# Optimization experiments

Hardware: AMD Instinct MI355X
Metric: run time of the kernel (lower is better)

The kernel has to match this reference:

```python
import jax, jax.numpy as jnp
import numpy as np

B, T, D_MODEL = 2, 2048, 2048
N_HEAD, N_KV, HD = 32, 8, 64


def _rope_tables(T, hd, base=10000.0):
    # standard rotary tables, (T, hd) with frequencies repeated over both halves
    inv_freq = 1.0 / (base ** (np.arange(0, hd // 2, dtype=np.float32) / (hd // 2)))
    t = np.arange(T, dtype=np.float32)
    freqs = np.outer(t, inv_freq)            # (T, hd/2)
    emb = np.concatenate([freqs, freqs], axis=-1)  # (T, hd)
    return jnp.asarray(np.cos(emb)), jnp.asarray(np.sin(emb))


def setup_inputs() -> dict:
    key = jax.random.key(0)
    ks = jax.random.split(key, 5)
    cos, sin = _rope_tables(T, HD)
    s = 0.02
    return {
        "x": jax.random.normal(ks[0], (B, T, D_MODEL), jnp.float32),
        "cos": cos,
        "sin": sin,
        "Wq": jax.random.normal(ks[1], (N_HEAD * HD, D_MODEL), jnp.float32) * s,
        "Wk": jax.random.normal(ks[2], (N_KV * HD, D_MODEL), jnp.float32) * s,
        "Wv": jax.random.normal(ks[3], (N_KV * HD, D_MODEL), jnp.float32) * s,
        "Wo": jax.random.normal(ks[4], (D_MODEL, N_HEAD * HD), jnp.float32) * s,
    }


def _apply_rope(x, cos, sin):
    # x: (B, H, T, D); cos/sin: (T, D)
    D = x.shape[-1]
    x1, x2 = x[..., : D // 2], x[..., D // 2 :]
    rot = jnp.concatenate([-x2, x1], axis=-1)
    c = cos[: x.shape[-2]][None, None]
    s = sin[: x.shape[-2]][None, None]
    return x * c + rot * s


def reference(x, cos, sin, Wq, Wk, Wv, Wo):
    Bv, Tv, _ = x.shape
    q = (x @ Wq.T).reshape(Bv, Tv, N_HEAD, HD).transpose(0, 2, 1, 3)  # (B,H,T,D)
    k = (x @ Wk.T).reshape(Bv, Tv, N_KV, HD).transpose(0, 2, 1, 3)    # (B,Hkv,T,D)
    v = (x @ Wv.T).reshape(Bv, Tv, N_KV, HD).transpose(0, 2, 1, 3)
    q = _apply_rope(q, cos, sin)
    k = _apply_rope(k, cos, sin)
    repeat = N_HEAD // N_KV
    if repeat > 1:
        k = jnp.repeat(k, repeat, axis=1)
        v = jnp.repeat(v, repeat, axis=1)
    scale = 1.0 / jnp.sqrt(jnp.float32(HD)).astype(x.dtype)
    scores = jnp.einsum("bhqd,bhkd->bhqk", q, k) * scale
    causal = jnp.tril(jnp.ones((Tv, Tv), dtype=bool))
    scores = jnp.where(causal[None, None], scores, jnp.finfo(scores.dtype).min)
    attn = jax.nn.softmax(scores, axis=-1)
    out = jnp.einsum("bhqk,bhkd->bhqd", attn, v)
    out = out.transpose(0, 2, 1, 3).reshape(Bv, Tv, N_HEAD * HD)
    return out @ Wo.T
```

## Files before the change

kernel.cpp:

```cpp
#include <hip/hip_runtime.h>
#include <stdint.h>

#define B_SZ 2
#define T_SEQ 2048
#define DM 2048
#define NH 32
#define NKV 8
#define HD 64
#define QKV_W 3072

typedef unsigned short u16;
typedef __bf16 bf16x8 __attribute__((ext_vector_type(8)));
typedef float floatx4 __attribute__((ext_vector_type(4)));

__device__ __forceinline__ float bf2f(u16 u) {
  union { unsigned u; float f; } v; v.u = ((unsigned)u) << 16; return v.f;
}
__device__ __forceinline__ u16 f2bf(float f) {
  union { float f; unsigned u; } v; v.f = f;
  unsigned r = v.u + 0x7fff + ((v.u >> 16) & 1);
  return (u16)(r >> 16);
}
__device__ __forceinline__ unsigned pk2bf(float hi, float lo) {
  return __builtin_amdgcn_perm(__float_as_uint(hi), __float_as_uint(lo), 0x07060302u);
}
__device__ __forceinline__ float fexp2(float x) {
#if __has_builtin(__builtin_amdgcn_exp2f)
  return __builtin_amdgcn_exp2f(x);
#else
  return exp2f(x);
#endif
}

__device__ __forceinline__ void gld_lds16(const void* g, void* l) {
  __builtin_amdgcn_global_load_lds(
      (const __attribute__((address_space(1))) unsigned int*)g,
      (__attribute__((address_space(3))) unsigned int*)l, 16, 0, 0);
}

__global__ __launch_bounds__(256) void conv_kernel(
    const float* __restrict__ src, u16* __restrict__ dst, int n4)
{
  int i = blockIdx.x * 256 + threadIdx.x;
  int stride = gridDim.x * 256;
  for (; i < n4; i += stride) {
    float4 v = ((const float4*)src)[i];
    ushort4 o;
    o.x = f2bf(v.x); o.y = f2bf(v.y); o.z = f2bf(v.z); o.w = f2bf(v.w);
    ((ushort4*)dst)[i] = o;
  }
}

__global__ __launch_bounds__(256) void gemm_qkv_kernel(
    const u16* __restrict__ A, const u16* __restrict__ Bt,
    u16* __restrict__ C)
{
  __shared__ __align__(16) u16 sA[128 * 32];
  __shared__ __align__(16) u16 sB[128 * 32];

  const int n0 = blockIdx.x * 128;
  const int m0 = blockIdx.y * 128;
  const int K = 2048;

  const int tid  = threadIdx.x;
  const int lane = tid & 63;
  const int w    = tid >> 6;
  const int wm = w >> 1, wn = w & 1;
  const int lm = lane & 15, lq = lane >> 4;

  floatx4 acc[4][4];
  #pragma unroll
  for (int i = 0; i < 4; i++)
    #pragma unroll
    for (int j = 0; j < 4; j++) { floatx4 z = {0.f,0.f,0.f,0.f}; acc[i][j] = z; }

  const int ar = tid >> 2;
  const int ac = (tid & 3) * 8;
  const u16* Ap0 = A  + (size_t)(m0 + ar) * K + ac;
  const u16* Ap1 = A  + (size_t)(m0 + 64 + ar) * K + ac;
  const u16* Bp0 = Bt + (size_t)(n0 + ar) * K + ac;
  const u16* Bp1 = Bt + (size_t)(n0 + 64 + ar) * K + ac;
  u16* sAd = sA + tid * 8;
  u16* sBd = sB + tid * 8;

  for (int k0 = 0; k0 < K; k0 += 32) {
    gld_lds16(Ap0 + k0, sAd);
    gld_lds16(Ap1 + k0, sAd + 2048);
    gld_lds16(Bp0 + k0, sBd);
    gld_lds16(Bp1 + k0, sBd + 2048);
    __syncthreads();

    bf16x8 af[4], bfr[4];
    #pragma unroll
    for (int mi = 0; mi < 4; mi++)
      af[mi] = *(const bf16x8*)(sA + (wm*64 + mi*16 + lm)*32 + lq*8);
    #pragma unroll
    for (int ni = 0; ni < 4; ni++)
      bfr[ni] = *(const bf16x8*)(sB + (wn*64 + ni*16 + lm)*32 + lq*8);

    #pragma unroll
    for (int mi = 0; mi < 4; mi++)
      #pragma unroll
      for (int ni = 0; ni < 4; ni++)
        acc[mi][ni] = __builtin_amdgcn_mfma_f32_16x16x32_bf16(
            af[mi], bfr[ni], acc[mi][ni], 0, 0, 0);
    __syncthreads();
  }

  #pragma unroll
  for (int mi = 0; mi < 4; mi++)
    #pragma unroll
    for (int ni = 0; ni < 4; ni++)
      #pragma unroll
      for (int r = 0; r < 4; r++) {
        int row = m0 + wm*64 + mi*16 + lq*4 + r;
        int col = n0 + wn*64 + ni*16 + lm;
        C[(size_t)row * QKV_W + col] = f2bf(acc[mi][ni][r]);
      }
}

__global__ __launch_bounds__(256) void gemm_out_kernel(
    const u16* __restrict__ A, const u16* __restrict__ Bt,
    float* __restrict__ C)
{
  __shared__ __align__(16) u16 sA[128 * 32];
  __shared__ __align__(16) u16 sB[128 * 32];

  const int n0 = blockIdx.x * 128;
  const int m0 = blockIdx.y * 128;
  const int K = 2048;

  const int tid  = threadIdx.x;
  const int lane = tid & 63;
  const int w    = tid >> 6;
  const int wm = w >> 1, wn = w & 1;
  const int lm = lane & 15, lq = lane >> 4;

  floatx4 acc[4][4];
  #pragma unroll
  for (int i = 0; i < 4; i++)
    #pragma unroll
    for (int j = 0; j < 4; j++) { floatx4 z = {0.f,0.f,0.f,0.f}; acc[i][j] = z; }

  const int ar = tid >> 2;
  const int ac = (tid & 3) * 8;
  const u16* Ap0 = A  + (size_t)(m0 + ar) * K + ac;
  const u16* Ap1 = A  + (size_t)(m0 + 64 + ar) * K + ac;
  const u16* Bp0 = Bt + (size_t)(n0 + ar) * K + ac;
  const u16* Bp1 = Bt + (size_t)(n0 + 64 + ar) * K + ac;
  u16* sAd = sA + tid * 8;
  u16* sBd = sB + tid * 8;

  for (int k0 = 0; k0 < K; k0 += 32) {
    gld_lds16(Ap0 + k0, sAd);
    gld_lds16(Ap1 + k0, sAd + 2048);
    gld_lds16(Bp0 + k0, sBd);
    gld_lds16(Bp1 + k0, sBd + 2048);
    __syncthreads();

    bf16x8 af[4], bfr[4];
    #pragma unroll
    for (int mi = 0; mi < 4; mi++)
      af[mi] = *(const bf16x8*)(sA + (wm*64 + mi*16 + lm)*32 + lq*8);
    #pragma unroll
    for (int ni = 0; ni < 4; ni++)
      bfr[ni] = *(const bf16x8*)(sB + (wn*64 + ni*16 + lm)*32 + lq*8);

    #pragma unroll
    for (int mi = 0; mi < 4; mi++)
      #pragma unroll
      for (int ni = 0; ni < 4; ni++)
        acc[mi][ni] = __builtin_amdgcn_mfma_f32_16x16x32_bf16(
            af[mi], bfr[ni], acc[mi][ni], 0, 0, 0);
    __syncthreads();
  }

  #pragma unroll
  for (int mi = 0; mi < 4; mi++)
    #pragma unroll
    for (int ni = 0; ni < 4; ni++)
      #pragma unroll
      for (int r = 0; r < 4; r++) {
        int row = m0 + wm*64 + mi*16 + lq*4 + r;
        int col = n0 + wn*64 + ni*16 + lm;
        C[(size_t)row * DM + col] = acc[mi][ni][r];
      }
}

#define QSCALE 0.180336880f
__global__ __launch_bounds__(256) void rope_kernel(
    const u16* __restrict__ qkv, const float* __restrict__ cosf,
    const float* __restrict__ sinf, u16* __restrict__ qb, u16* __restrict__ kb)
{
  const int bt = blockIdx.x;
  const int b = bt / T_SEQ, t = bt % T_SEQ;
  const int tid = threadIdx.x;
  const u16* row = qkv + (size_t)bt * QKV_W;

  #pragma unroll
  for (int i = 0; i < 4; i++) {
    int idx = i * 256 + tid;
    int h = idx >> 5, dp = idx & 31;
    float x1 = bf2f(row[h * 64 + dp]);
    float x2 = bf2f(row[h * 64 + dp + 32]);
    float c = cosf[t * 64 + dp];
    float s = sinf[t * 64 + dp];
    float o1 = (x1 * c - x2 * s) * QSCALE;
    float o2 = (x2 * c + x1 * s) * QSCALE;
    size_t base = ((size_t)(b * NH + h) * T_SEQ + t) * HD + dp;
    qb[base]      = f2bf(o1);
    qb[base + 32] = f2bf(o2);
  }
  {
    int idx = tid;
    int kvh = idx >> 5, dp = idx & 31;
    float x1 = bf2f(row[2048 + kvh * 64 + dp]);
    float x2 = bf2f(row[2048 + kvh * 64 + dp + 32]);
    float c = cosf[t * 64 + dp];
    float s = sinf[t * 64 + dp];
    size_t base = ((size_t)(b * NKV + kvh) * T_SEQ + t) * HD + dp;
    kb[base]      = f2bf(x1 * c - x2 * s);
    kb[base + 32] = f2bf(x2 * c + x1 * s);
  }
}

__global__ __launch_bounds__(256) void vtrans_kernel(
    const u16* __restrict__ qkv, u16* __restrict__ vbt)
{
  __shared__ u16 tile[64][66];
  const int t0  = blockIdx.x * 64;
  const int kvh = blockIdx.y;
  const int b   = blockIdx.z;
  const int tid = threadIdx.x;

  #pragma unroll
  for (int i = 0; i < 16; i++) {
    int idx = i * 256 + tid;
    int r = idx >> 6, c = idx & 63;
    tile[r][c] = qkv[(size_t)(b * T_SEQ + t0 + r) * QKV_W + 2560 + kvh * 64 + c];
  }
  __syncthreads();
  #pragma unroll
  for (int i = 0; i < 16; i++) {
    int idx = i * 256 + tid;
    int d = idx >> 6, c = idx & 63;
    vbt[((size_t)(b * NKV + kvh) * HD + d) * T_SEQ + t0 + c] = tile[c][d];
  }
}

__global__ __launch_bounds__(256, 3) void attn_kernel(
    const u16* __restrict__ qb, const u16* __restrict__ kb,
    const u16* __restrict__ vbt, u16* __restrict__ attn)
{
  __shared__ __align__(16) u16 sK[2][64 * 64];
  __shared__ __align__(16) u16 sV[2][64 * 64];
  __shared__ __align__(16) u16 sP[4][16][72];
  __shared__ float sAl[4][16];

  const int tid  = threadIdx.x;
  const int lane = tid & 63;
  const int w    = tid >> 6;

  const int l  = blockIdx.x;
  const int qt = 63 - (l >> 4);
  const int kv = l & 7;
  const int b  = (l >> 3) & 1;
  const int h  = kv * 4 + w;
  const int ktmax = qt >> 1;
  const int moff  = 32 * (qt & 1);

  const int lm = lane & 15, lq = lane >> 4;
  const int sw = lm & 7;

  bf16x8 qf[2][2];
  {
    const u16* qhead = qb + ((size_t)(b * NH + h) * T_SEQ + qt * 32) * HD;
    #pragma unroll
    for (int nq = 0; nq < 2; nq++) {
      const u16* qrow = qhead + (size_t)(nq * 16 + lm) * HD + lq * 8;
      qf[nq][0] = *(const bf16x8*)(qrow);
      qf[nq][1] = *(const bf16x8*)(qrow + 32);
    }
  }

  floatx4 o_acc[2][4];
  #pragma unroll
  for (int i = 0; i < 2; i++)
    #pragma unroll
    for (int j = 0; j < 4; j++) { floatx4 z = {0.f,0.f,0.f,0.f}; o_acc[i][j] = z; }
  float m_run[2] = {-1e30f, -1e30f};
  float l_run[2] = {0.f, 0.f};

  const u16* kbase = kb  + (size_t)(b * NKV + kv) * T_SEQ * HD;
  const u16* vbase = vbt + (size_t)(b * NKV + kv) * HD * T_SEQ;

  const int p0row = tid >> 3,        p1row = (256 + tid) >> 3;
  const int p0ck  = (tid & 7) ^ (p0row & 7), p1ck = ((256 + tid) & 7) ^ (p1row & 7);
  const u16* kp0 = kbase + (size_t)p0row * HD + p0ck * 8;
  const u16* kp1 = kbase + (size_t)p1row * HD + p1ck * 8;
  const u16* vp0 = vbase + (size_t)p0row * T_SEQ + p0ck * 8;
  const u16* vp1 = vbase + (size_t)p1row * T_SEQ + p1ck * 8;
  char* sKb = (char*)sK;
  char* sVb = (char*)sV;
  const int d0 = tid * 16, d1 = (256 + tid) * 16;

  gld_lds16(kp0, sKb + d0);
  gld_lds16(kp1, sKb + d1);
  gld_lds16(vp0, sVb + d0);
  gld_lds16(vp1, sVb + d1);

  for (int kt = 0; kt <= ktmax; kt++) {
    __syncthreads();
    const int cur = kt & 1;
    if (kt < ktmax) {
      const int nb = (cur ^ 1) * 8192;
      const size_t ko = (size_t)(kt + 1) * 64 * HD;
      const int vo = (kt + 1) * 64;
      gld_lds16(kp0 + ko, sKb + nb + d0);
      gld_lds16(kp1 + ko, sKb + nb + d1);
      gld_lds16(vp0 + vo, sVb + nb + d0);
      gld_lds16(vp1 + vo, sVb + nb + d1);
    }
    const u16* sKc = sK[cur];
    const u16* sVc = sV[cur];

    bf16x8 kf[4][2], vf[4][2];
    #pragma unroll
    for (int nt = 0; nt < 4; nt++) {
      kf[nt][0] = *(const bf16x8*)(sKc + (((nt*16 + lm) * 8 + (lq ^ sw)) << 3));
      kf[nt][1] = *(const bf16x8*)(sKc + (((nt*16 + lm) * 8 + ((4 + lq) ^ sw)) << 3));
      vf[nt][0] = *(const bf16x8*)(sVc + (((nt*16 + lm) * 8 + (lq ^ sw)) << 3));
      vf[nt][1] = *(const bf16x8*)(sVc + (((nt*16 + lm) * 8 + ((4 + lq) ^ sw)) << 3));
    }

    #pragma unroll
    for (int nq = 0; nq < 2; nq++) {
      floatx4 s_acc[4];
      __builtin_amdgcn_s_setprio(1);
      #pragma unroll
      for (int nt = 0; nt < 4; nt++) {
        floatx4 z = {0.f,0.f,0.f,0.f};
        z = __builtin_amdgcn_mfma_f32_16x16x32_bf16(kf[nt][0], qf[nq][0], z, 0, 0, 0);
        z = __builtin_amdgcn_mfma_f32_16x16x32_bf16(kf[nt][1], qf[nq][1], z, 0, 0, 0);
        s_acc[nt] = z;
      }
      __builtin_amdgcn_s_setprio(0);

      if (kt == ktmax) {
        #pragma unroll
        for (int nt = 0; nt < 4; nt++)
          #pragma unroll
          for (int r = 0; r < 4; r++)
            if (nt * 16 + lq * 4 + r > nq * 16 + lm + moff) s_acc[nt][r] = -1e30f;
      }

      float mloc = s_acc[0][0];
      #pragma unroll
      for (int nt = 0; nt < 4; nt++)
        #pragma unroll
        for (int r = 0; r < 4; r++) mloc = fmaxf(mloc, s_acc[nt][r]);
      mloc = fmaxf(mloc, __shfl_xor(mloc, 16));
      mloc = fmaxf(mloc, __shfl_xor(mloc, 32));

      float mnew = m_run[nq];
      if (!__all(mloc - m_run[nq] <= 8.0f)) {
        mnew = fmaxf(m_run[nq], mloc);
        float al = fexp2(m_run[nq] - mnew);
        m_run[nq] = mnew;
        l_run[nq] *= al;
        if (lq == 0) sAl[w][lm] = al;
        floatx4 alv = *(const floatx4*)&sAl[w][lq * 4];
        #pragma unroll
        for (int nd = 0; nd < 4; nd++)
          #pragma unroll
          for (int r = 0; r < 4; r++)
            o_acc[nq][nd][r] *= alv[r];
      }

      float rs = 0.f;
      uint2 pk[4];
      #pragma unroll
      for (int nt = 0; nt < 4; nt++) {
        float p0 = fexp2(s_acc[nt][0] - mnew);
        float p1 = fexp2(s_acc[nt][1] - mnew);
        float p2 = fexp2(s_acc[nt][2] - mnew);
        float p3 = fexp2(s_acc[nt][3] - mnew);
        rs += (p0 + p1) + (p2 + p3);
        pk[nt].x = pk2bf(p1, p0);
        pk[nt].y = pk2bf(p3, p2);
      }
      rs += __shfl_xor(rs, 16);
      rs += __shfl_xor(rs, 32);
      l_run[nq] += rs;

      #pragma unroll
      for (int nt = 0; nt < 4; nt++)
        *(uint2*)&sP[w][lm][nt * 16 + lq * 4] = pk[nt];

      __builtin_amdgcn_s_setprio(1);
      #pragma unroll
      for (int st = 0; st < 2; st++) {
        bf16x8 pf = *(const bf16x8*)(&sP[w][lm][st * 32 + lq * 8]);
        #pragma unroll
        for (int nd = 0; nd < 4; nd++)
          o_acc[nq][nd] = __builtin_amdgcn_mfma_f32_16x16x32_bf16(
              pf, vf[nd][st], o_acc[nq][nd], 0, 0, 0);
      }
      __builtin_amdgcn_s_setprio(0);
    }
  }

  #pragma unroll
  for (int nq = 0; nq < 2; nq++) {
    __builtin_amdgcn_s_waitcnt(0);
    if (lq == 0) sAl[w][lm] = l_run[nq];
    floatx4 lv = *(const floatx4*)&sAl[w][lq * 4];
    #pragma unroll
    for (int nd = 0; nd < 4; nd++)
      #pragma unroll
      for (int r = 0; r < 4; r++) {
        float v = o_acc[nq][nd][r] / lv[r];
        size_t row = (size_t)b * T_SEQ + qt * 32 + nq * 16 + lq * 4 + r;
        attn[row * DM + h * HD + nd * 16 + lm] = f2bf(v);
      }
  }
}

extern "C" void kernel_launch(void* const* d_in, const int* in_sizes, int n_in,
                              void* d_out, int out_size, void* d_ws, size_t ws_size,
                              hipStream_t stream)
{
  const float* x    = (const float*)d_in[0];
  const float* cosf = (const float*)d_in[1];
  const float* sinf = (const float*)d_in[2];
  const float* Wq   = (const float*)d_in[3];
  const float* Wk   = (const float*)d_in[4];
  const float* Wv   = (const float*)d_in[5];
  const float* Wo   = (const float*)d_in[6];
  float* out = (float*)d_out;

  char* ws = (char*)d_ws;
  u16* qkvb  = (u16*)(ws + 0);
  u16* attnb = (u16*)(ws + 0);
  u16* qb    = (u16*)(ws + 25165824);
  u16* kb    = (u16*)(ws + 41943040);
  u16* vbt   = (u16*)(ws + 46137344);
  u16* xb    = (u16*)(ws + 50331648);
  u16* wob   = (u16*)(ws + 50331648);
  u16* wqkvb = (u16*)(ws + 67108864);

  dim3 blk(256);
  conv_kernel<<<dim3(2048), blk, 0, stream>>>(x,  xb,                 8388608 / 4);
  conv_kernel<<<dim3(1024), blk, 0, stream>>>(Wq, wqkvb,              4194304 / 4);
  conv_kernel<<<dim3(512),  blk, 0, stream>>>(Wk, wqkvb + 2048*2048,  1048576 / 4);
  conv_kernel<<<dim3(512),  blk, 0, stream>>>(Wv, wqkvb + 2560*2048,  1048576 / 4);

  gemm_qkv_kernel<<<dim3(24, 32), blk, 0, stream>>>(xb, wqkvb, qkvb);

  conv_kernel<<<dim3(1024), blk, 0, stream>>>(Wo, wob, 4194304 / 4);

  rope_kernel<<<dim3(B_SZ * T_SEQ), blk, 0, stream>>>(qkvb, cosf, sinf, qb, kb);
  vtrans_kernel<<<dim3(T_SEQ / 64, NKV, B_SZ), blk, 0, stream>>>(qkvb, vbt);
  attn_kernel<<<dim3(1024), blk, 0, stream>>>(qb, kb, vbt, attnb);
  gemm_out_kernel<<<dim3(16, 32), blk, 0, stream>>>(attnb, wob, out);
}
```

Measured before the change: 311.2 us.

## Double-buffer LDS tiles in both GEMMs and merge QKV weight conversions

Both projection GEMMs now use two LDS buffers and issue the async global-to-LDS loads for the next K slice before computing on the current one. This removes one barrier per iteration and overlaps load latency with MFMA work. The three weight conversion launches for Wq, Wk and Wv are merged into a single kernel to cut launch overhead. LDS use per block doubles, which could lower occupancy. Because only a barrier guards the asynchronous loads, correctness depends on the global_load_lds completion semantics at that barrier.

Result: slower. 318.6 us (+2.4%).

```diff
diff --git a/kernel.cpp b/kernel.cpp
--- a/kernel.cpp
+++ b/kernel.cpp
@@ -51,12 +51,29 @@
   }
 }
 
+__global__ __launch_bounds__(256) void conv_wqkv_kernel(
+    const float* __restrict__ Wq, const float* __restrict__ Wk,
+    const float* __restrict__ Wv, u16* __restrict__ dst)
+{
+  int i = blockIdx.x * 256 + threadIdx.x;
+  int stride = gridDim.x * 256;
+  for (; i < 1572864; i += stride) {
+    float4 v;
+    if (i < 1048576)      v = ((const float4*)Wq)[i];
+    else if (i < 1310720) v = ((const float4*)Wk)[i - 1048576];
+    else                  v = ((const float4*)Wv)[i - 1310720];
+    ushort4 o;
+    o.x = f2bf(v.x); o.y = f2bf(v.y); o.z = f2bf(v.z); o.w = f2bf(v.w);
+    ((ushort4*)dst)[i] = o;
+  }
+}
+
 __global__ __launch_bounds__(256) void gemm_qkv_kernel(
     const u16* __restrict__ A, const u16* __restrict__ Bt,
     u16* __restrict__ C)
 {
-  __shared__ __align__(16) u16 sA[128 * 32];
-  __shared__ __align__(16) u16 sB[128 * 32];
+  __shared__ __align__(16) u16 sA[2][128 * 32];
+  __shared__ __align__(16) u16 sB[2][128 * 32];
 
   const int n0 = blockIdx.x * 128;
   const int m0 = blockIdx.y * 128;
@@ -80,23 +97,34 @@
   const u16* Ap1 = A  + (size_t)(m0 + 64 + ar) * K + ac;
   const u16* Bp0 = Bt + (size_t)(n0 + ar) * K + ac;
   const u16* Bp1 = Bt + (size_t)(n0 + 64 + ar) * K + ac;
-  u16* sAd = sA + tid * 8;
-  u16* sBd = sB + tid * 8;
-
-  for (int k0 = 0; k0 < K; k0 += 32) {
-    gld_lds16(Ap0 + k0, sAd);
-    gld_lds16(Ap1 + k0, sAd + 2048);
-    gld_lds16(Bp0 + k0, sBd);
-    gld_lds16(Bp1 + k0, sBd + 2048);
+  u16* sAd = sA[0] + tid * 8;
+  u16* sBd = sB[0] + tid * 8;
+
+  gld_lds16(Ap0, sAd);
+  gld_lds16(Ap1, sAd + 2048);
+  gld_lds16(Bp0, sBd);
+  gld_lds16(Bp1, sBd + 2048);
+
+  for (int k0 = 0, t = 0; k0 < K; k0 += 32, ++t) {
     __syncthreads();
+    const int cur = t & 1;
+    if (k0 + 32 < K) {
+      const int nb = (cur ^ 1) * 4096;
+      gld_lds16(Ap0 + k0 + 32, sAd + nb);
+      gld_lds16(Ap1 + k0 + 32, sAd + nb + 2048);
+      gld_lds16(Bp0 + k0 + 32, sBd + nb);
+      gld_lds16(Bp1 + k0 + 32, sBd + nb + 2048);
+    }
+    const u16* sAc = sA[cur];
+    const u16* sBc = sB[cur];
 
     bf16x8 af[4], bfr[4];
     #pragma unroll
     for (int mi = 0; mi < 4; mi++)
-      af[mi] = *(const bf16x8*)(sA + (wm*64 + mi*16 + lm)*32 + lq*8);
+      af[mi] = *(const bf16x8*)(sAc + (wm*64 + mi*16 + lm)*32 + lq*8);
     #pragma unroll
     for (int ni = 0; ni < 4; ni++)
-      bfr[ni] = *(const bf16x8*)(sB + (wn*64 + ni*16 + lm)*32 + lq*8);
+      bfr[ni] = *(const bf16x8*)(sBc + (wn*64 + ni*16 + lm)*32 + lq*8);
 
     #pragma unroll
     for (int mi = 0; mi < 4; mi++)
@@ -104,7 +132,6 @@
       for (int ni = 0; ni < 4; ni++)
         acc[mi][ni] = __builtin_amdgcn_mfma_f32_16x16x32_bf16(
             af[mi], bfr[ni], acc[mi][ni], 0, 0, 0);
-    __syncthreads();
   }
 
   #pragma unroll
@@ -123,8 +150,8 @@
     const u16* __restrict__ A, const u16* __restrict__ Bt,
     float* __restrict__ C)
 {
-  __shared__ __align__(16) u16 sA[128 * 32];
-  __shared__ __align__(16) u16 sB[128 * 32];
+  __shared__ __align__(16) u16 sA[2][128 * 32];
+  __shared__ __align__(16) u16 sB[2][128 * 32];
 
   const int n0 = blockIdx.x * 128;
   const int m0 = blockIdx.y * 128;
@@ -148,23 +175,34 @@
   const u16* Ap1 = A  + (size_t)(m0 + 64 + ar) * K + ac;
   const u16* Bp0 = Bt + (size_t)(n0 + ar) * K + ac;
   const u16* Bp1 = Bt + (size_t)(n0 + 64 + ar) * K + ac;
-  u16* sAd = sA + tid * 8;
-  u16* sBd = sB + tid * 8;
-
-  for (int k0 = 0; k0 < K; k0 += 32) {
-    gld_lds16(Ap0 + k0, sAd);
-    gld_lds16(Ap1 + k0, sAd + 2048);
-    gld_lds16(Bp0 + k0, sBd);
-    gld_lds16(Bp1 + k0, sBd + 2048);
+  u16* sAd = sA[0] + tid * 8;
+  u16* sBd = sB[0] + tid * 8;
+
+  gld_lds16(Ap0, sAd);
+  gld_lds16(Ap1, sAd + 2048);
+  gld_lds16(Bp0, sBd);
+  gld_lds16(Bp1, sBd + 2048);
+
+  for (int k0 = 0, t = 0; k0 < K; k0 += 32, ++t) {
     __syncthreads();
+    const int cur = t & 1;
+    if (k0 + 32 < K) {
+      const int nb = (cur ^ 1) * 4096;
+      gld_lds16(Ap0 + k0 + 32, sAd + nb);
+      gld_lds16(Ap1 + k0 + 32, sAd + nb + 2048);
+      gld_lds16(Bp0 + k0 + 32, sBd + nb);
+      gld_lds16(Bp1 + k0 + 32, sBd + nb + 2048);
+    }
+    const u16* sAc = sA[cur];
+    const u16* sBc = sB[cur];
 
     bf16x8 af[4], bfr[4];
     #pragma unroll
     for (int mi = 0; mi < 4; mi++)
-      af[mi] = *(const bf16x8*)(sA + (wm*64 + mi*16 + lm)*32 + lq*8);
+      af[mi] = *(const bf16x8*)(sAc + (wm*64 + mi*16 + lm)*32 + lq*8);
     #pragma unroll
     for (int ni = 0; ni < 4; ni++)
-      bfr[ni] = *(const bf16x8*)(sB + (wn*64 + ni*16 + lm)*32 + lq*8);
+      bfr[ni] = *(const bf16x8*)(sBc + (wn*64 + ni*16 + lm)*32 + lq*8);
 
     #pragma unroll
     for (int mi = 0; mi < 4; mi++)
@@ -172,7 +210,6 @@
       for (int ni = 0; ni < 4; ni++)
         acc[mi][ni] = __builtin_amdgcn_mfma_f32_16x16x32_bf16(
             af[mi], bfr[ni], acc[mi][ni], 0, 0, 0);
-    __syncthreads();
   }
 
   #pragma unroll
@@ -450,10 +487,8 @@
   u16* wqkvb = (u16*)(ws + 67108864);
 
   dim3 blk(256);
-  conv_kernel<<<dim3(2048), blk, 0, stream>>>(x,  xb,                 8388608 / 4);
-  conv_kernel<<<dim3(1024), blk, 0, stream>>>(Wq, wqkvb,              4194304 / 4);
-  conv_kernel<<<dim3(512),  blk, 0, stream>>>(Wk, wqkvb + 2048*2048,  1048576 / 4);
-  conv_kernel<<<dim3(512),  blk, 0, stream>>>(Wv, wqkvb + 2560*2048,  1048576 / 4);
+  conv_kernel<<<dim3(2048), blk, 0, stream>>>(x, xb, 8388608 / 4);
+  conv_wqkv_kernel<<<dim3(1536), blk, 0, stream>>>(Wq, Wk, Wv, wqkvb);
 
   gemm_qkv_kernel<<<dim3(24, 32), blk, 0, stream>>>(xb, wqkvb, qkvb);
 
```
